# Optimization experiments

Hardware: AMD Instinct MI355X
Metric: run time of the kernel (lower is better)

The kernel has to match this reference:

```python
import jax, jax.numpy as jnp
import numpy as np

EPS = 1e-5

def layer_norm(x, w, b):
    mu = jnp.mean(x, axis=-1, keepdims=True)
    var = jnp.mean(jnp.square(x - mu), axis=-1, keepdims=True)
    return (x - mu) * jax.lax.rsqrt(var + EPS) * w + b

def setup_inputs() -> dict:
    key = jax.random.key(0)
    ks = jax.random.split(key, 12)
    B, T, C = 4, 2048, 1024
    s = lambda d: 1.0 / np.sqrt(d)
    return {
        "x":      jax.random.normal(ks[0], (B, T, C), dtype=jnp.float32),
        "w_attn": jax.random.normal(ks[1], (C, 3 * C), dtype=jnp.float32) * s(C),
        "b_attn": jnp.zeros((3 * C,), jnp.float32),
        "w_o":    jax.random.normal(ks[2], (C, C), dtype=jnp.float32) * s(C),
        "b_o":    jnp.zeros((C,), jnp.float32),
        "ln_w":   jnp.ones((C,), jnp.float32),
        "ln_b":   jnp.zeros((C,), jnp.float32),
        "w_fc1":  jax.random.normal(ks[3], (C, 4 * C), dtype=jnp.float32) * s(C),
        "b_fc1":  jnp.zeros((4 * C,), jnp.float32),
        "w_fc2":  jax.random.normal(ks[4], (4 * C, C), dtype=jnp.float32) * s(4 * C),
        "b_fc2":  jnp.zeros((C,), jnp.float32),
        "n_heads": 16,
    }

def reference(x, w_attn, b_attn, w_o, b_o, ln_w, ln_b, w_fc1, b_fc1, w_fc2, b_fc2, n_heads):
    B, T, C = x.shape
    H = n_heads
    Dh = C // H
    qkv = x @ w_attn + b_attn                      # [B,T,3C]
    q, k, v = jnp.split(qkv, 3, axis=-1)
    q = q.reshape(B, T, H, Dh).transpose(0, 2, 1, 3)  # [B,H,T,Dh]
    k = k.reshape(B, T, H, Dh).transpose(0, 2, 1, 3)
    v = v.reshape(B, T, H, Dh).transpose(0, 2, 1, 3)
    scores = jnp.einsum("bhtd,bhsd->bhts", q, k) / jnp.sqrt(jnp.float32(Dh))
    w = jax.nn.softmax(scores, axis=-1)            # no causal mask in source
    out = jnp.einsum("bhts,bhsd->bhtd", w, v)      # [B,H,T,Dh]
    out = out.transpose(0, 2, 1, 3).reshape(B, T, C)
    attn_out = out @ w_o + b_o
    x = x + attn_out
    h = layer_norm(x, ln_w, ln_b)
    h = jax.nn.gelu(h @ w_fc1 + b_fc1, approximate=False)
    h = h @ w_fc2 + b_fc2
    return x + h
```

## Files before the change

kernel.cpp:

```cpp
#include <hip/hip_runtime.h>
#include <hip/hip_bf16.h>
#include <math.h>
#include <stdint.h>

typedef __attribute__((ext_vector_type(8))) short s16x8;
typedef __attribute__((ext_vector_type(4))) float f32x4;
typedef __attribute__((ext_vector_type(4))) u_int32_t u32x4;
typedef unsigned int u32;
typedef unsigned short u16;

#define DEVINL __device__ __forceinline__

DEVINL u16 f2bf(float f) {
    u32 b = __builtin_bit_cast(u32, f);
    u32 r = (b + 0x7fffu + ((b >> 16) & 1u)) >> 16;
    return (u16)r;
}

DEVINL float fexp2(float x) {
    float r;
    asm("v_exp_f32 %0, %1" : "=v"(r) : "v"(x));
    return r;
}

DEVINL u32 cvt_pk_bf16(float lo, float hi) {
    u32 r;
    asm("v_cvt_pk_bf16_f32 %0, %1, %2" : "=v"(r) : "v"(lo), "v"(hi));
    return r;
}

DEVINL void gload_lds16(const void* g, const void* l) {
    __builtin_amdgcn_global_load_lds(
        (const __attribute__((address_space(1))) u32*)(uintptr_t)g,
        (__attribute__((address_space(3))) u32*)(uintptr_t)l, 16, 0, 0);
}

__global__ __launch_bounds__(256)
void cvt_bf16_kernel(const float* __restrict__ in, u16* __restrict__ out, int n4)
{
    int i = blockIdx.x * 256 + threadIdx.x;
    const int stride = gridDim.x * 256;
    for (; i < n4; i += stride) {
        float4 v = ((const float4*)in)[i];
        ushort4 o;
        o.x = f2bf(v.x); o.y = f2bf(v.y); o.z = f2bf(v.z); o.w = f2bf(v.w);
        ((ushort4*)out)[i] = o;
    }
}

__global__ __launch_bounds__(256)
void transpose_cvt(const float* __restrict__ src, u16* __restrict__ dst, int R, int C)
{
    __shared__ float tile[64][65];
    const int t = threadIdx.x;
    const int c0 = blockIdx.x * 64, r0 = blockIdx.y * 64;
    const int rr = t >> 6;
    const int cc = t & 63;
    #pragma unroll
    for (int i = 0; i < 16; ++i)
        tile[i * 4 + rr][cc] = src[(size_t)(r0 + i * 4 + rr) * C + c0 + cc];
    __syncthreads();
    #pragma unroll
    for (int i = 0; i < 16; ++i) {
        int orow = i * 4 + rr;
        dst[(size_t)(c0 + orow) * R + r0 + cc] = f2bf(tile[cc][orow]);
    }
}

__global__ __launch_bounds__(256)
void vtrans_kernel(const u16* __restrict__ qkv, u16* __restrict__ vt)
{
    __shared__ u16 tile[64][68];
    const int t = threadIdx.x;
    const int st = blockIdx.x;
    const int bh = blockIdx.y;
    const int b = bh >> 4, h = bh & 15;
    const int s0 = st * 64;
    const int rr = t >> 6, cc = t & 63;
    const int sc = (cc & 32) | (((cc >> 2) & 3) << 3) | (((cc >> 4) & 1) << 2) | (cc & 3);
    #pragma unroll
    for (int i = 0; i < 16; ++i) {
        int s = i * 4 + rr;
        tile[s][cc] = qkv[(size_t)(b * 2048 + s0 + s) * 3072 + 2048 + h * 64 + cc];
    }
    __syncthreads();
    #pragma unroll
    for (int i = 0; i < 16; ++i) {
        int d = i * 4 + rr;
        vt[(size_t)(bh * 64 + d) * 2048 + s0 + sc] = tile[cc][d];
    }
}

template<int BM, int MODE, int QSC>
__global__ __launch_bounds__(512, 1)
void gemm8p(const u16* __restrict__ A, const u16* __restrict__ B,
            const float* __restrict__ bias, const float* __restrict__ resid,
            u16* __restrict__ obf, float* __restrict__ of32,
            int M, int N, int K)
{
    constexpr int MF = BM / 32;
    constexpr int NPH = MF / 2;
    constexpr int ALOADS = BM / 64;
    constexpr int ABYTES = BM * 128;
    constexpr int BUFBYTES = ABYTES + 32768;
    extern __shared__ char lds[];

    const int t = threadIdx.x;
    const int lane = t & 63, w = t >> 6;
    const int wr = w >> 2, wc = w & 3;
    const int g = lane >> 4, lr = lane & 15;
    const int bm = blockIdx.x * BM, bn = blockIdx.y * 256;

    const int srow = t >> 3;
    const int scol = (((t & 7) ^ (srow & 7)) * 8);
    const u16* ag = A + (size_t)(bm + srow) * K + scol;
    const u16* bg = B + (size_t)(bn + srow) * K + scol;

    f32x4 acc[MF][4] = {};

    #pragma unroll
    for (int L = 0; L < ALOADS; ++L)
        gload_lds16(ag + (size_t)L * 64 * K, lds + L * 8192 + t * 16);
    #pragma unroll
    for (int L = 0; L < 4; ++L)
        gload_lds16(bg + (size_t)L * 64 * K, lds + ABYTES + L * 8192 + t * 16);
    __syncthreads();

    const int NK = K >> 6;
    const int xr = (lr & 7) << 4;

    for (int h = 0; h < NK; ++h) {
        char* cbuf = lds + (h & 1) * BUFBYTES;
        char* nbuf = lds + ((h + 1) & 1) * BUFBYTES;

        if (h + 1 < NK) {
            const size_t ko = (size_t)(h + 1) * 64;
            #pragma unroll
            for (int L = 0; L < ALOADS; ++L)
                gload_lds16(ag + (size_t)L * 64 * K + ko, nbuf + L * 8192 + t * 16);
            #pragma unroll
            for (int L = 0; L < 4; ++L)
                gload_lds16(bg + (size_t)L * 64 * K + ko, nbuf + ABYTES + L * 8192 + t * 16);
        }

        s16x8 bf[4][2];
        #pragma unroll
        for (int nf = 0; nf < 4; ++nf) {
            const int brow = wc * 64 + nf * 16 + lr;
            #pragma unroll
            for (int ks = 0; ks < 2; ++ks)
                bf[nf][ks] = *(const s16x8*)(cbuf + ABYTES + brow * 128 + ((ks * 64 + g * 16) ^ xr));
        }

        #pragma unroll
        for (int p = 0; p < NPH; ++p) {
            s16x8 af[2][2];
            #pragma unroll
            for (int mi = 0; mi < 2; ++mi) {
                const int arow = wr * (BM / 2) + (p * 2 + mi) * 16 + lr;
                #pragma unroll
                for (int ks = 0; ks < 2; ++ks)
                    af[mi][ks] = *(const s16x8*)(cbuf + arow * 128 + ((ks * 64 + g * 16) ^ xr));
            }
            __builtin_amdgcn_sched_barrier(0);
            __builtin_amdgcn_s_barrier();
            __builtin_amdgcn_s_setprio(1);
            #pragma unroll
            for (int ks = 0; ks < 2; ++ks)
                #pragma unroll
                for (int mi = 0; mi < 2; ++mi)
                    #pragma unroll
                    for (int nf = 0; nf < 4; ++nf)
                        acc[p * 2 + mi][nf] = __builtin_amdgcn_mfma_f32_16x16x32_bf16(
                            af[mi][ks], bf[nf][ks], acc[p * 2 + mi][nf], 0, 0, 0);
            __builtin_amdgcn_s_setprio(0);
            __builtin_amdgcn_sched_barrier(0);
            if (p < NPH - 1) __builtin_amdgcn_s_barrier();
            else __syncthreads();
        }
    }

    #pragma unroll
    for (int mf = 0; mf < MF; ++mf) {
        const int rbase = bm + wr * (BM / 2) + mf * 16 + g * 4;
        #pragma unroll
        for (int nf = 0; nf < 4; ++nf) {
            const int col = bn + wc * 64 + nf * 16 + lr;
            const float bia = bias[col];
            #pragma unroll
            for (int b2 = 0; b2 < 4; ++b2) {
                const int r = rbase + b2;
                float v = acc[mf][nf][b2] + bia;
                if (QSC && col < 1024) v *= 0.18033688011112042f;
                if (MODE == 1) v = 0.5f * v * (1.0f + erff(v * 0.70710678118654752f));
                if (MODE == 2) {
                    v += resid[(size_t)r * N + col];
                    of32[(size_t)r * N + col] = v;
                } else {
                    obf[(size_t)r * N + col] = f2bf(v);
                }
            }
        }
    }
}

__global__ __launch_bounds__(256)
void attn_kernel(const u16* __restrict__ qkv, const u16* __restrict__ vt,
                 u16* __restrict__ attnb)
{
    __shared__ u16 Kls[2][4096];
    __shared__ u16 Vls[2][4096];
    const int t = threadIdx.x, lane = t & 63, w = t >> 6;
    const int g = lane >> 4, lr = lane & 15;
    const int wg = blockIdx.x;
    const int xcd = wg & 7, slot = wg >> 3;
    const int bh = xcd * 8 + (slot >> 5);
    const int qt = slot & 31;
    const int b = bh >> 4, h = bh & 15;

    const int srow = t >> 3;
    const int scol = (((t & 7) ^ (srow & 7)) * 8);
    const u16* kg0 = qkv + (size_t)(b * 2048 + srow) * 3072 + 1024 + h * 64 + scol;
    const u16* kg1 = qkv + (size_t)(b * 2048 + srow + 32) * 3072 + 1024 + h * 64 + scol;
    const u16* vg0 = vt + (size_t)(bh * 64 + srow) * 2048 + scol;
    const u16* vg1 = vt + (size_t)(bh * 64 + srow + 32) * 2048 + scol;
    const int ldst = w * 512;

    gload_lds16(kg0, &Kls[0][ldst]);
    gload_lds16(kg1, &Kls[0][2048 + ldst]);
    gload_lds16(vg0, &Vls[0][ldst]);
    gload_lds16(vg1, &Vls[0][2048 + ldst]);

    const int qtok = b * 2048 + qt * 64 + w * 16 + lr;
    const u16* qp = qkv + (size_t)qtok * 3072 + h * 64;
    const s16x8 qf0 = *(const s16x8*)(qp + g * 8);
    const s16x8 qf1 = *(const s16x8*)(qp + 32 + g * 8);

    f32x4 o[4] = {};
    float psum = 0.f;
    const int xr = (lr & 7) * 8;

    for (int s = 0; s < 32; ++s) {
        const int cur = s & 1;
        __syncthreads();
        if (s + 1 < 32) {
            const size_t ko = (size_t)(s + 1) * 64;
            gload_lds16(kg0 + ko * 3072, &Kls[cur ^ 1][ldst]);
            gload_lds16(kg1 + ko * 3072, &Kls[cur ^ 1][2048 + ldst]);
            gload_lds16(vg0 + ko, &Vls[cur ^ 1][ldst]);
            gload_lds16(vg1 + ko, &Vls[cur ^ 1][2048 + ldst]);
        }

        f32x4 sv[4];
        #pragma unroll
        for (int n = 0; n < 4; ++n) {
            const int kr = (n * 16 + lr) * 64;
            const s16x8 k0v = *(const s16x8*)&Kls[cur][kr + ((g * 8) ^ xr)];
            const s16x8 k1v = *(const s16x8*)&Kls[cur][kr + ((32 + g * 8) ^ xr)];
            f32x4 z = {};
            z = __builtin_amdgcn_mfma_f32_16x16x32_bf16(k0v, qf0, z, 0, 0, 0);
            z = __builtin_amdgcn_mfma_f32_16x16x32_bf16(k1v, qf1, z, 0, 0, 0);
            sv[n] = z;
        }

        float p[4][4];
        #pragma unroll
        for (int n = 0; n < 4; ++n) {
            #pragma unroll
            for (int b2 = 0; b2 < 4; ++b2)
                p[n][b2] = fexp2(sv[n][b2]);
            psum += (p[n][0] + p[n][1]) + (p[n][2] + p[n][3]);
        }

        u32x4 pk0, pk1;
        pk0[0] = cvt_pk_bf16(p[0][0], p[0][1]);
        pk0[1] = cvt_pk_bf16(p[0][2], p[0][3]);
        pk0[2] = cvt_pk_bf16(p[1][0], p[1][1]);
        pk0[3] = cvt_pk_bf16(p[1][2], p[1][3]);
        pk1[0] = cvt_pk_bf16(p[2][0], p[2][1]);
        pk1[1] = cvt_pk_bf16(p[2][2], p[2][3]);
        pk1[2] = cvt_pk_bf16(p[3][0], p[3][1]);
        pk1[3] = cvt_pk_bf16(p[3][2], p[3][3]);
        const s16x8 pa0 = __builtin_bit_cast(s16x8, pk0);
        const s16x8 pa1 = __builtin_bit_cast(s16x8, pk1);

        #pragma unroll
        for (int n = 0; n < 4; ++n) {
            const int vr = (n * 16 + lr) * 64;
            const s16x8 v0 = *(const s16x8*)&Vls[cur][vr + ((g * 8) ^ xr)];
            const s16x8 v1 = *(const s16x8*)&Vls[cur][vr + ((32 + g * 8) ^ xr)];
            o[n] = __builtin_amdgcn_mfma_f32_16x16x32_bf16(pa0, v0, o[n], 0, 0, 0);
            o[n] = __builtin_amdgcn_mfma_f32_16x16x32_bf16(pa1, v1, o[n], 0, 0, 0);
        }
    }

    psum += __shfl_xor(psum, 16);
    psum += __shfl_xor(psum, 32);
    const int orow0 = b * 2048 + qt * 64 + w * 16 + g * 4;
    #pragma unroll
    for (int b2 = 0; b2 < 4; ++b2) {
        const float inv = 1.0f / __shfl(psum, g * 4 + b2);
        #pragma unroll
        for (int n = 0; n < 4; ++n)
            attnb[(size_t)(orow0 + b2) * 1024 + h * 64 + n * 16 + lr] = f2bf(o[n][b2] * inv);
    }
}

__global__ __launch_bounds__(256)
void ln_kernel(const float* __restrict__ x, const float* __restrict__ lw,
               const float* __restrict__ lb, u16* __restrict__ out)
{
    const int row = blockIdx.x;
    const int t = threadIdx.x;
    const float4 v = ((const float4*)(x + (size_t)row * 1024))[t];
    float s = v.x + v.y + v.z + v.w;
    float s2 = v.x * v.x + v.y * v.y + v.z * v.z + v.w * v.w;
    #pragma unroll
    for (int m = 32; m >= 1; m >>= 1) {
        s  += __shfl_xor(s, m);
        s2 += __shfl_xor(s2, m);
    }
    __shared__ float red[16];
    const int w = t >> 6, lane = t & 63;
    if (lane == 0) { red[w] = s; red[8 + w] = s2; }
    __syncthreads();
    s  = red[0] + red[1] + red[2] + red[3];
    s2 = red[8] + red[9] + red[10] + red[11];
    const float mu = s * (1.0f / 1024.0f);
    const float var = s2 * (1.0f / 1024.0f) - mu * mu;
    const float inv = rsqrtf(var + 1e-5f);
    const float4 wv = ((const float4*)lw)[t];
    const float4 bv = ((const float4*)lb)[t];
    ushort4 oo;
    oo.x = f2bf((v.x - mu) * inv * wv.x + bv.x);
    oo.y = f2bf((v.y - mu) * inv * wv.y + bv.y);
    oo.z = f2bf((v.z - mu) * inv * wv.z + bv.z);
    oo.w = f2bf((v.w - mu) * inv * wv.w + bv.w);
    ((ushort4*)(out + (size_t)row * 1024))[t] = oo;
}

extern "C" void kernel_launch(void* const* d_in, const int* in_sizes, int n_in,
                              void* d_out, int out_size, void* d_ws, size_t ws_size,
                              hipStream_t stream)
{
    const float* x      = (const float*)d_in[0];
    const float* w_attn = (const float*)d_in[1];
    const float* b_attn = (const float*)d_in[2];
    const float* w_o    = (const float*)d_in[3];
    const float* b_o    = (const float*)d_in[4];
    const float* ln_w   = (const float*)d_in[5];
    const float* ln_b   = (const float*)d_in[6];
    const float* w_fc1  = (const float*)d_in[7];
    const float* b_fc1  = (const float*)d_in[8];
    const float* w_fc2  = (const float*)d_in[9];
    const float* b_fc2  = (const float*)d_in[10];
    float* out = (float*)d_out;

    char* ws = (char*)d_ws;
    u16*   xb    = (u16*)(ws);
    u16*   wqkvT = (u16*)(ws + 16777216);
    u16*   woT   = (u16*)(ws + 23068672);
    u16*   w1T   = (u16*)(ws + 25165824);
    u16*   w2T   = (u16*)(ws + 33554432);
    float* x1    = (float*)(ws + 41943040);
    u16*   attnb = (u16*)(ws + 75497472);
    u16*   hb    = attnb;
    u16*   qkvb  = (u16*)(ws + 92274688);
    u16*   vtb   = qkvb + 25165824;
    u16*   h1    = qkvb;

    cvt_bf16_kernel<<<2048, 256, 0, stream>>>(x, xb, 8192 * 1024 / 4);
    transpose_cvt<<<dim3(48, 16), 256, 0, stream>>>(w_attn, wqkvT, 1024, 3072);
    transpose_cvt<<<dim3(16, 16), 256, 0, stream>>>(w_o,   woT,  1024, 1024);
    transpose_cvt<<<dim3(64, 16), 256, 0, stream>>>(w_fc1, w1T,  1024, 4096);
    transpose_cvt<<<dim3(16, 64), 256, 0, stream>>>(w_fc2, w2T,  4096, 1024);

    gemm8p<128, 0, 1><<<dim3(64, 12), 512, 98304, stream>>>(xb, wqkvT, b_attn, nullptr,
                                                            qkvb, nullptr, 8192, 3072, 1024);
    vtrans_kernel<<<dim3(32, 64), 256, 0, stream>>>(qkvb, vtb);
    attn_kernel<<<2048, 256, 0, stream>>>(qkvb, vtb, attnb);
    gemm8p<128, 2, 0><<<dim3(64, 4), 512, 98304, stream>>>(attnb, woT, b_o, x,
                                                           nullptr, x1, 8192, 1024, 1024);
    ln_kernel<<<8192, 256, 0, stream>>>(x1, ln_w, ln_b, hb);
    gemm8p<256, 1, 0><<<dim3(32, 16), 512, 131072, stream>>>(hb, w1T, b_fc1, nullptr,
                                                             h1, nullptr, 8192, 4096, 1024);
    gemm8p<128, 2, 0><<<dim3(64, 4), 512, 98304, stream>>>(h1, w2T, b_fc2, x1,
                                                           nullptr, out, 8192, 1024, 4096);
}
```

Baseline: 416.1 us.

## Replace double-buffered GEMM with 4-stage K=32 pipeline and swizzled block order

Rewrites the bf16 MFMA GEMM to use four LDS stages of K=32 each with three tiles in flight, gated by explicit vmcnt waits and a single barrier per step. The old version double-buffered K=64 tiles and needed several barriers per tile. The change also remaps the 1-D grid with an XCD-style swizzle to improve L2 reuse across blocks. The intent is to hide global-load latency better and cut synchronisation overhead. In exchange, each barrier now covers less MFMA work, and the hand-written vmcnt counts must match the number of loads issued exactly.

```diff
diff --git a/kernel.cpp b/kernel.cpp
--- a/kernel.cpp
+++ b/kernel.cpp
@@ -10,6 +10,7 @@
 typedef unsigned short u16;
 
 #define DEVINL __device__ __forceinline__
+#define VMW(n) asm volatile("s_waitcnt vmcnt(" #n ")" ::: "memory")
 
 DEVINL u16 f2bf(float f) {
     u32 b = __builtin_bit_cast(u32, f);
@@ -93,91 +94,80 @@
 
 template<int BM, int MODE, int QSC>
 __global__ __launch_bounds__(512, 1)
-void gemm8p(const u16* __restrict__ A, const u16* __restrict__ B,
+void gemm4s(const u16* __restrict__ A, const u16* __restrict__ B,
             const float* __restrict__ bias, const float* __restrict__ resid,
             u16* __restrict__ obf, float* __restrict__ of32,
-            int M, int N, int K)
+            int M, int N, int K, int NMB)
 {
     constexpr int MF = BM / 32;
-    constexpr int NPH = MF / 2;
-    constexpr int ALOADS = BM / 64;
-    constexpr int ABYTES = BM * 128;
-    constexpr int BUFBYTES = ABYTES + 32768;
+    constexpr int LA = BM / 128;
+    constexpr int LPT = LA + 2;
+    constexpr int ABYTES = BM * 64;
+    constexpr int BUF = ABYTES + 16384;
     extern __shared__ char lds[];
 
-    const int t = threadIdx.x;
-    const int lane = t & 63, w = t >> 6;
-    const int wr = w >> 2, wc = w & 3;
-    const int g = lane >> 4, lr = lane & 15;
-    const int bm = blockIdx.x * BM, bn = blockIdx.y * 256;
-
-    const int srow = t >> 3;
-    const int scol = (((t & 7) ^ (srow & 7)) * 8);
+    const int t = threadIdx.x, lane = t & 63, w = t >> 6;
+    const int wr = w >> 2, wc = w & 3, g = lane >> 4, lr = lane & 15;
+
+    const int wg = blockIdx.x;
+    const int swz = (wg & 7) * (gridDim.x >> 3) + (wg >> 3);
+    const int mb = swz % NMB, nb = swz / NMB;
+    const int bm = mb * BM, bn = nb * 256;
+
+    const int srow = t >> 2;
+    const int scol = ((t & 3) ^ (srow & 3)) * 8;
     const u16* ag = A + (size_t)(bm + srow) * K + scol;
     const u16* bg = B + (size_t)(bn + srow) * K + scol;
 
     f32x4 acc[MF][4] = {};
 
-    #pragma unroll
-    for (int L = 0; L < ALOADS; ++L)
-        gload_lds16(ag + (size_t)L * 64 * K, lds + L * 8192 + t * 16);
-    #pragma unroll
-    for (int L = 0; L < 4; ++L)
-        gload_lds16(bg + (size_t)L * 64 * K, lds + ABYTES + L * 8192 + t * 16);
-    __syncthreads();
-
-    const int NK = K >> 6;
-    const int xr = (lr & 7) << 4;
-
-    for (int h = 0; h < NK; ++h) {
-        char* cbuf = lds + (h & 1) * BUFBYTES;
-        char* nbuf = lds + ((h + 1) & 1) * BUFBYTES;
-
-        if (h + 1 < NK) {
-            const size_t ko = (size_t)(h + 1) * 64;
-            #pragma unroll
-            for (int L = 0; L < ALOADS; ++L)
-                gload_lds16(ag + (size_t)L * 64 * K + ko, nbuf + L * 8192 + t * 16);
-            #pragma unroll
-            for (int L = 0; L < 4; ++L)
-                gload_lds16(bg + (size_t)L * 64 * K + ko, nbuf + ABYTES + L * 8192 + t * 16);
-        }
-
-        s16x8 bf[4][2];
+    auto STAGE = [&](int tt) {
+        char* bb = lds + (tt & 3) * BUF;
+        const size_t ko = (size_t)tt * 32;
+        #pragma unroll
+        for (int L = 0; L < LA; ++L)
+            gload_lds16(ag + (size_t)L * 128 * K + ko, bb + L * 8192 + t * 16);
+        #pragma unroll
+        for (int L = 0; L < 2; ++L)
+            gload_lds16(bg + (size_t)L * 128 * K + ko, bb + ABYTES + L * 8192 + t * 16);
+    };
+
+    const int NT = K >> 5;
+    STAGE(0); STAGE(1); STAGE(2);
+
+    const int xun = (lr & 3) << 4;
+
+    for (int tt = 0; tt < NT; ++tt) {
+        const int rem = NT - 1 - tt;
+        if constexpr (LPT == 4) {
+            if (rem >= 2) { VMW(8); } else if (rem == 1) { VMW(4); } else { VMW(0); }
+        } else {
+            if (rem >= 2) { VMW(6); } else if (rem == 1) { VMW(3); } else { VMW(0); }
+        }
+        __builtin_amdgcn_s_barrier();
+        asm volatile("" ::: "memory");
+        if (tt + 3 < NT) STAGE(tt + 3);
+
+        char* cbuf = lds + (tt & 3) * BUF;
+        s16x8 af[MF], bf4[4];
+        #pragma unroll
+        for (int mf = 0; mf < MF; ++mf) {
+            const int arow = wr * (BM / 2) + mf * 16 + lr;
+            af[mf] = *(const s16x8*)(cbuf + arow * 64 + ((g * 16) ^ xun));
+        }
         #pragma unroll
         for (int nf = 0; nf < 4; ++nf) {
             const int brow = wc * 64 + nf * 16 + lr;
+            bf4[nf] = *(const s16x8*)(cbuf + ABYTES + brow * 64 + ((g * 16) ^ xun));
+        }
+        __builtin_amdgcn_s_setprio(1);
+        #pragma unroll
+        for (int mf = 0; mf < MF; ++mf)
             #pragma unroll
-            for (int ks = 0; ks < 2; ++ks)
-                bf[nf][ks] = *(const s16x8*)(cbuf + ABYTES + brow * 128 + ((ks * 64 + g * 16) ^ xr));
-        }
-
-        #pragma unroll
-        for (int p = 0; p < NPH; ++p) {
-            s16x8 af[2][2];
-            #pragma unroll
-            for (int mi = 0; mi < 2; ++mi) {
-                const int arow = wr * (BM / 2) + (p * 2 + mi) * 16 + lr;
-                #pragma unroll
-                for (int ks = 0; ks < 2; ++ks)
-                    af[mi][ks] = *(const s16x8*)(cbuf + arow * 128 + ((ks * 64 + g * 16) ^ xr));
-            }
-            __builtin_amdgcn_sched_barrier(0);
-            __builtin_amdgcn_s_barrier();
-            __builtin_amdgcn_s_setprio(1);
-            #pragma unroll
-            for (int ks = 0; ks < 2; ++ks)
-                #pragma unroll
-                for (int mi = 0; mi < 2; ++mi)
-                    #pragma unroll
-                    for (int nf = 0; nf < 4; ++nf)
-                        acc[p * 2 + mi][nf] = __builtin_amdgcn_mfma_f32_16x16x32_bf16(
-                            af[mi][ks], bf[nf][ks], acc[p * 2 + mi][nf], 0, 0, 0);
-            __builtin_amdgcn_s_setprio(0);
-            __builtin_amdgcn_sched_barrier(0);
-            if (p < NPH - 1) __builtin_amdgcn_s_barrier();
-            else __syncthreads();
-        }
+            for (int nf = 0; nf < 4; ++nf)
+                acc[mf][nf] = __builtin_amdgcn_mfma_f32_16x16x32_bf16(
+                    af[mf], bf4[nf], acc[mf][nf], 0, 0, 0);
+        __builtin_amdgcn_s_setprio(0);
     }
 
     #pragma unroll
@@ -375,15 +365,15 @@
     transpose_cvt<<<dim3(64, 16), 256, 0, stream>>>(w_fc1, w1T,  1024, 4096);
     transpose_cvt<<<dim3(16, 64), 256, 0, stream>>>(w_fc2, w2T,  4096, 1024);
 
-    gemm8p<128, 0, 1><<<dim3(64, 12), 512, 98304, stream>>>(xb, wqkvT, b_attn, nullptr,
-                                                            qkvb, nullptr, 8192, 3072, 1024);
+    gemm4s<128, 0, 1><<<768, 512, 98304, stream>>>(xb, wqkvT, b_attn, nullptr,
+                                                   qkvb, nullptr, 8192, 3072, 1024, 64);
     vtrans_kernel<<<dim3(32, 64), 256, 0, stream>>>(qkvb, vtb);
     attn_kernel<<<2048, 256, 0, stream>>>(qkvb, vtb, attnb);
-    gemm8p<128, 2, 0><<<dim3(64, 4), 512, 98304, stream>>>(attnb, woT, b_o, x,
-                                                           nullptr, x1, 8192, 1024, 1024);
+    gemm4s<128, 2, 0><<<256, 512, 98304, stream>>>(attnb, woT, b_o, x,
+                                                   nullptr, x1, 8192, 1024, 1024, 64);
     ln_kernel<<<8192, 256, 0, stream>>>(x1, ln_w, ln_b, hb);
-    gemm8p<256, 1, 0><<<dim3(32, 16), 512, 131072, stream>>>(hb, w1T, b_fc1, nullptr,
-                                                             h1, nullptr, 8192, 4096, 1024);
-    gemm8p<128, 2, 0><<<dim3(64, 4), 512, 98304, stream>>>(h1, w2T, b_fc2, x1,
-                                                           nullptr, out, 8192, 1024, 4096);
-}
+    gemm4s<256, 1, 0><<<512, 512, 131072, stream>>>(hb, w1T, b_fc1, nullptr,
+                                                    h1, nullptr, 8192, 4096, 1024, 32);
+    gemm4s<128, 2, 0><<<256, 512, 98304, stream>>>(h1, w2T, b_fc2, x1,
+                                                   nullptr, out, 8192, 1024, 4096, 64);
+}
```

After: 449.6 us. 8.0% more time.

## Replace double-buffered GEMM with three-stage LDS pipeline using vmcnt waits

Applied to the files above, without the earlier changes.

Rewrites the bf16 MFMA GEMM to use a three-slot LDS ring with two tiles prefetched ahead, waiting on vmcnt counters and a single barrier per K step instead of per-phase barriers and a full syncthreads. All A fragments are loaded up front and the MFMA block runs in one pass. The FC1 GEMM drops its 256-row tile for the uniform 128-row tile, doubling its grid. The aim is to hide global-load latency better and cut barrier overhead, at the cost of more LDS per block (144KB) and more register pressure.

```diff
diff --git a/kernel.cpp b/kernel.cpp
--- a/kernel.cpp
+++ b/kernel.cpp
@@ -10,6 +10,7 @@
 typedef unsigned short u16;
 
 #define DEVINL __device__ __forceinline__
+#define VMW(n) asm volatile("s_waitcnt vmcnt(" #n ")" ::: "memory")
 
 DEVINL u16 f2bf(float f) {
     u32 b = __builtin_bit_cast(u32, f);
@@ -91,98 +92,81 @@
     }
 }
 
-template<int BM, int MODE, int QSC>
+template<int MODE, int QSC>
 __global__ __launch_bounds__(512, 1)
-void gemm8p(const u16* __restrict__ A, const u16* __restrict__ B,
+void gemm3s(const u16* __restrict__ A, const u16* __restrict__ B,
             const float* __restrict__ bias, const float* __restrict__ resid,
             u16* __restrict__ obf, float* __restrict__ of32,
             int M, int N, int K)
 {
-    constexpr int MF = BM / 32;
-    constexpr int NPH = MF / 2;
-    constexpr int ALOADS = BM / 64;
-    constexpr int ABYTES = BM * 128;
-    constexpr int BUFBYTES = ABYTES + 32768;
+    constexpr int ABYTES = 128 * 128;
+    constexpr int BUF = ABYTES + 32768;
     extern __shared__ char lds[];
 
-    const int t = threadIdx.x;
-    const int lane = t & 63, w = t >> 6;
-    const int wr = w >> 2, wc = w & 3;
-    const int g = lane >> 4, lr = lane & 15;
-    const int bm = blockIdx.x * BM, bn = blockIdx.y * 256;
+    const int t = threadIdx.x, lane = t & 63, w = t >> 6;
+    const int wr = w >> 2, wc = w & 3, g = lane >> 4, lr = lane & 15;
+    const int bm = blockIdx.x * 128, bn = blockIdx.y * 256;
 
     const int srow = t >> 3;
     const int scol = (((t & 7) ^ (srow & 7)) * 8);
     const u16* ag = A + (size_t)(bm + srow) * K + scol;
     const u16* bg = B + (size_t)(bn + srow) * K + scol;
 
-    f32x4 acc[MF][4] = {};
-
-    #pragma unroll
-    for (int L = 0; L < ALOADS; ++L)
-        gload_lds16(ag + (size_t)L * 64 * K, lds + L * 8192 + t * 16);
-    #pragma unroll
-    for (int L = 0; L < 4; ++L)
-        gload_lds16(bg + (size_t)L * 64 * K, lds + ABYTES + L * 8192 + t * 16);
-    __syncthreads();
-
-    const int NK = K >> 6;
+    f32x4 acc[4][4] = {};
+
+    auto STAGE = [&](int tt) {
+        char* bb = lds + (tt % 3) * BUF;
+        const size_t ko = (size_t)tt * 64;
+        #pragma unroll
+        for (int L = 0; L < 2; ++L)
+            gload_lds16(ag + (size_t)L * 64 * K + ko, bb + L * 8192 + t * 16);
+        #pragma unroll
+        for (int L = 0; L < 4; ++L)
+            gload_lds16(bg + (size_t)L * 64 * K + ko, bb + ABYTES + L * 8192 + t * 16);
+    };
+
+    const int NT = K >> 6;
+    STAGE(0); STAGE(1);
+
     const int xr = (lr & 7) << 4;
 
-    for (int h = 0; h < NK; ++h) {
-        char* cbuf = lds + (h & 1) * BUFBYTES;
-        char* nbuf = lds + ((h + 1) & 1) * BUFBYTES;
-
-        if (h + 1 < NK) {
-            const size_t ko = (size_t)(h + 1) * 64;
-            #pragma unroll
-            for (int L = 0; L < ALOADS; ++L)
-                gload_lds16(ag + (size_t)L * 64 * K + ko, nbuf + L * 8192 + t * 16);
-            #pragma unroll
-            for (int L = 0; L < 4; ++L)
-                gload_lds16(bg + (size_t)L * 64 * K + ko, nbuf + ABYTES + L * 8192 + t * 16);
-        }
-
-        s16x8 bf[4][2];
+    for (int tt = 0; tt < NT; ++tt) {
+        if (tt < NT - 1) { VMW(6); } else { VMW(0); }
+        __builtin_amdgcn_s_barrier();
+        asm volatile("" ::: "memory");
+        if (tt + 2 < NT) STAGE(tt + 2);
+
+        const char* cbuf = lds + (tt % 3) * BUF;
+        s16x8 af[4][2], bf4[4][2];
+        #pragma unroll
+        for (int mf = 0; mf < 4; ++mf) {
+            const int arow = wr * 64 + mf * 16 + lr;
+            #pragma unroll
+            for (int ks = 0; ks < 2; ++ks)
+                af[mf][ks] = *(const s16x8*)(cbuf + arow * 128 + ((ks * 64 + g * 16) ^ xr));
+        }
         #pragma unroll
         for (int nf = 0; nf < 4; ++nf) {
             const int brow = wc * 64 + nf * 16 + lr;
             #pragma unroll
             for (int ks = 0; ks < 2; ++ks)
-                bf[nf][ks] = *(const s16x8*)(cbuf + ABYTES + brow * 128 + ((ks * 64 + g * 16) ^ xr));
-        }
-
-        #pragma unroll
-        for (int p = 0; p < NPH; ++p) {
-            s16x8 af[2][2];
-            #pragma unroll
-            for (int mi = 0; mi < 2; ++mi) {
-                const int arow = wr * (BM / 2) + (p * 2 + mi) * 16 + lr;
+                bf4[nf][ks] = *(const s16x8*)(cbuf + ABYTES + brow * 128 + ((ks * 64 + g * 16) ^ xr));
+        }
+        __builtin_amdgcn_s_setprio(1);
+        #pragma unroll
+        for (int ks = 0; ks < 2; ++ks)
+            #pragma unroll
+            for (int mf = 0; mf < 4; ++mf)
                 #pragma unroll
-                for (int ks = 0; ks < 2; ++ks)
-                    af[mi][ks] = *(const s16x8*)(cbuf + arow * 128 + ((ks * 64 + g * 16) ^ xr));
-            }
-            __builtin_amdgcn_sched_barrier(0);
-            __builtin_amdgcn_s_barrier();
-            __builtin_amdgcn_s_setprio(1);
-            #pragma unroll
-            for (int ks = 0; ks < 2; ++ks)
-                #pragma unroll
-                for (int mi = 0; mi < 2; ++mi)
-                    #pragma unroll
-                    for (int nf = 0; nf < 4; ++nf)
-                        acc[p * 2 + mi][nf] = __builtin_amdgcn_mfma_f32_16x16x32_bf16(
-                            af[mi][ks], bf[nf][ks], acc[p * 2 + mi][nf], 0, 0, 0);
-            __builtin_amdgcn_s_setprio(0);
-            __builtin_amdgcn_sched_barrier(0);
-            if (p < NPH - 1) __builtin_amdgcn_s_barrier();
-            else __syncthreads();
-        }
-    }
-
-    #pragma unroll
-    for (int mf = 0; mf < MF; ++mf) {
-        const int rbase = bm + wr * (BM / 2) + mf * 16 + g * 4;
+                for (int nf = 0; nf < 4; ++nf)
+                    acc[mf][nf] = __builtin_amdgcn_mfma_f32_16x16x32_bf16(
+                        af[mf][ks], bf4[nf][ks], acc[mf][nf], 0, 0, 0);
+        __builtin_amdgcn_s_setprio(0);
+    }
+
+    #pragma unroll
+    for (int mf = 0; mf < 4; ++mf) {
+        const int rbase = bm + wr * 64 + mf * 16 + g * 4;
         #pragma unroll
         for (int nf = 0; nf < 4; ++nf) {
             const int col = bn + wc * 64 + nf * 16 + lr;
@@ -375,15 +359,15 @@
     transpose_cvt<<<dim3(64, 16), 256, 0, stream>>>(w_fc1, w1T,  1024, 4096);
     transpose_cvt<<<dim3(16, 64), 256, 0, stream>>>(w_fc2, w2T,  4096, 1024);
 
-    gemm8p<128, 0, 1><<<dim3(64, 12), 512, 98304, stream>>>(xb, wqkvT, b_attn, nullptr,
-                                                            qkvb, nullptr, 8192, 3072, 1024);
+    gemm3s<0, 1><<<dim3(64, 12), 512, 147456, stream>>>(xb, wqkvT, b_attn, nullptr,
+                                                        qkvb, nullptr, 8192, 3072, 1024);
     vtrans_kernel<<<dim3(32, 64), 256, 0, stream>>>(qkvb, vtb);
     attn_kernel<<<2048, 256, 0, stream>>>(qkvb, vtb, attnb);
-    gemm8p<128, 2, 0><<<dim3(64, 4), 512, 98304, stream>>>(attnb, woT, b_o, x,
-                                                           nullptr, x1, 8192, 1024, 1024);
+    gemm3s<2, 0><<<dim3(64, 4), 512, 147456, stream>>>(attnb, woT, b_o, x,
+                                                       nullptr, x1, 8192, 1024, 1024);
     ln_kernel<<<8192, 256, 0, stream>>>(x1, ln_w, ln_b, hb);
-    gemm8p<256, 1, 0><<<dim3(32, 16), 512, 131072, stream>>>(hb, w1T, b_fc1, nullptr,
-                                                             h1, nullptr, 8192, 4096, 1024);
-    gemm8p<128, 2, 0><<<dim3(64, 4), 512, 98304, stream>>>(h1, w2T, b_fc2, x1,
-                                                           nullptr, out, 8192, 1024, 4096);
-}
+    gemm3s<1, 0><<<dim3(64, 16), 512, 147456, stream>>>(hb, w1T, b_fc1, nullptr,
+                                                        h1, nullptr, 8192, 4096, 1024);
+    gemm3s<2, 0><<<dim3(64, 4), 512, 147456, stream>>>(h1, w2T, b_fc2, x1,
+                                                       nullptr, out, 8192, 1024, 4096);
+}
```

Result: no change. 417.0 us (+0.2%).
